# Kernel optimization log

Measured on AMD Instinct MI355X. Metric: run time of the kernel, lower is better.

## Reference

```python
import jax, jax.numpy as jnp
import numpy as np

N_QUBITS = 2
N_LAYERS = 2
EPS = 1e-12  # tf.math.l2_normalize epsilon


def _apply_rx(state, theta, wire):
    """Apply RX(theta) to `wire` of a batched 2-qubit state.
    state: [B,2,2] complex64 (axis1 = qubit0, axis2 = qubit1); theta: [B] float.
    RX(t) = [[cos(t/2), -i sin(t/2)], [-i sin(t/2), cos(t/2)]]
    """
    c = jnp.cos(theta * 0.5)[:, None].astype(state.dtype)
    s = (-1j * jnp.sin(theta * 0.5))[:, None].astype(state.dtype)
    if wire == 0:
        a, b = state[:, 0, :], state[:, 1, :]
        return jnp.stack([c * a + s * b, s * a + c * b], axis=1)
    else:
        a, b = state[:, :, 0], state[:, :, 1]
        return jnp.stack([c * a + s * b, s * a + c * b], axis=2)


def _cnot01(state):
    # CNOT control=0, target=1: flip qubit1 where qubit0 == 1
    return jnp.stack([state[:, 0, :], state[:, 1, ::-1]], axis=1)


def _circuit(angles, weights_q):
    """angles: [B,2] embedding angles; weights_q: [L,2]. Returns [B,2] <Z_i>."""
    B = angles.shape[0]
    state = jnp.zeros((B, 2, 2), dtype=jnp.complex64).at[:, 0, 0].set(1.0)
    # AngleEmbedding (RX rotations, one per wire)
    state = _apply_rx(state, angles[:, 0], 0)
    state = _apply_rx(state, angles[:, 1], 1)
    # BasicEntanglerLayers: RX per wire then single CNOT(0,1) for 2 wires
    for l in range(weights_q.shape[0]):
        state = _apply_rx(state, jnp.broadcast_to(weights_q[l, 0], (B,)), 0)
        state = _apply_rx(state, jnp.broadcast_to(weights_q[l, 1], (B,)), 1)
        state = _cnot01(state)
    probs = (state * jnp.conj(state)).real  # [B,2,2]
    z0 = probs[:, 0, :].sum(-1) - probs[:, 1, :].sum(-1)
    z1 = probs[:, :, 0].sum(-1) - probs[:, :, 1].sum(-1)
    return jnp.stack([z0, z1], axis=-1).astype(jnp.float32)


def setup_inputs() -> dict:
    key = jax.random.key(0)
    k1, k2, k3, k4 = jax.random.split(key, 4)
    B, D = 65536, 1024
    return {
        "x": jax.random.normal(k1, (B, D), dtype=jnp.float32),
        "dense_w": jax.random.normal(k2, (D, N_QUBITS), dtype=jnp.float32) * 0.05,
        "dense_b": jax.random.normal(k3, (N_QUBITS,), dtype=jnp.float32) * 0.05,
        "weights_q": jax.random.normal(k4, (N_LAYERS, N_QUBITS), dtype=jnp.float32) * 0.05,
    }


def reference(x, dense_w, dense_b, weights_q):
    h = x @ dense_w + dense_b  # [B,2]
    # tf.math.l2_normalize(h, axis=-1)
    h = h * jax.lax.rsqrt(jnp.maximum(jnp.sum(h * h, axis=-1, keepdims=True), EPS))
    return _circuit(h, weights_q)  # [B,2]
```

## Files before the change

### kernel.cpp

```cpp
#include <hip/hip_runtime.h>


#define WAVES_PER_BLOCK 4
#define ROWS_PER_WAVE   8
#define ROWS_PER_BLOCK  (WAVES_PER_BLOCK * ROWS_PER_WAVE)

__device__ __forceinline__ float2 run_circuit(float h0, float h1,
                                              const float cw[2][2],
                                              const float sw[2][2]) {
    float inv = rsqrtf(fmaxf(h0 * h0 + h1 * h1, 1e-12f));
    float s0, c0, s1, c1;
    __sincosf(0.5f * h0 * inv, &s0, &c0);
    __sincosf(0.5f * h1 * inv, &s1, &c1);

    float re[2][2], im[2][2];
    re[0][0] = c0 * c1;  im[0][0] = 0.0f;
    re[0][1] = 0.0f;     im[0][1] = -c0 * s1;
    re[1][0] = 0.0f;     im[1][0] = -s0 * c1;
    re[1][1] = -s0 * s1; im[1][1] = 0.0f;

#pragma unroll
    for (int l = 0; l < 2; ++l) {
        {
            float c = cw[l][0], s = sw[l][0];
#pragma unroll
            for (int k = 0; k < 2; ++k) {
                float ar = re[0][k], ai = im[0][k];
                float br = re[1][k], bi = im[1][k];
                re[0][k] = c * ar + s * bi;
                im[0][k] = c * ai - s * br;
                re[1][k] = s * ai + c * br;
                im[1][k] = c * bi - s * ar;
            }
        }
        {
            float c = cw[l][1], s = sw[l][1];
#pragma unroll
            for (int k = 0; k < 2; ++k) {
                float ar = re[k][0], ai = im[k][0];
                float br = re[k][1], bi = im[k][1];
                re[k][0] = c * ar + s * bi;
                im[k][0] = c * ai - s * br;
                re[k][1] = s * ai + c * br;
                im[k][1] = c * bi - s * ar;
            }
        }
        {
            float tr = re[1][0], ti = im[1][0];
            re[1][0] = re[1][1]; im[1][0] = im[1][1];
            re[1][1] = tr;       im[1][1] = ti;
        }
    }

    float p00 = re[0][0] * re[0][0] + im[0][0] * im[0][0];
    float p01 = re[0][1] * re[0][1] + im[0][1] * im[0][1];
    float p10 = re[1][0] * re[1][0] + im[1][0] * im[1][0];
    float p11 = re[1][1] * re[1][1] + im[1][1] * im[1][1];

    float2 z;
    z.x = (p00 + p01) - (p10 + p11);
    z.y = (p00 + p10) - (p01 + p11);
    return z;
}

__global__ __launch_bounds__(256) void qlayer_kernel(
    const float* __restrict__ x,
    const float* __restrict__ w,
    const float* __restrict__ bias,
    const float* __restrict__ wq,
    float* __restrict__ out,
    int B)
{
    const int lane = threadIdx.x & 63;
    const int wave = threadIdx.x >> 6;
    const int rowBase = (blockIdx.x * WAVES_PER_BLOCK + wave) * ROWS_PER_WAVE;
    if (rowBase >= B) return;

    const float4* __restrict__ w4 = (const float4*)w;
    float4 wA[4], wB[4];
#pragma unroll
    for (int j = 0; j < 4; ++j) {
        int f = lane + 64 * j;
        wA[j] = w4[2 * f];
        wB[j] = w4[2 * f + 1];
    }

    const float b0 = bias[0], b1 = bias[1];

    float cw[2][2], sw[2][2];
#pragma unroll
    for (int l = 0; l < 2; ++l) {
#pragma unroll
        for (int q = 0; q < 2; ++q) {
            float t = 0.5f * wq[l * 2 + q];
            __sincosf(t, &sw[l][q], &cw[l][q]);
        }
    }

    float2* __restrict__ out2 = (float2*)out;

#pragma unroll
    for (int r = 0; r < ROWS_PER_WAVE; r += 2) {
        const int rowA = rowBase + r;
        const int rowB = rowA + 1;
        const bool hasB = (rowB < B);
        if (rowA >= B) break;

        const float4* __restrict__ xA = (const float4*)x + (size_t)rowA * 256;
        const float4* __restrict__ xB = (const float4*)x + (size_t)(hasB ? rowB : rowA) * 256;

        float a0 = 0.f, a1 = 0.f, c0s = 0.f, c1s = 0.f;
#pragma unroll
        for (int j = 0; j < 4; ++j) {
            const int f = lane + 64 * j;
            float4 va = xA[f];
            float4 vb = xB[f];
            a0 = fmaf(va.x, wA[j].x, a0); a1 = fmaf(va.x, wA[j].y, a1);
            a0 = fmaf(va.y, wA[j].z, a0); a1 = fmaf(va.y, wA[j].w, a1);
            a0 = fmaf(va.z, wB[j].x, a0); a1 = fmaf(va.z, wB[j].y, a1);
            a0 = fmaf(va.w, wB[j].z, a0); a1 = fmaf(va.w, wB[j].w, a1);
            c0s = fmaf(vb.x, wA[j].x, c0s); c1s = fmaf(vb.x, wA[j].y, c1s);
            c0s = fmaf(vb.y, wA[j].z, c0s); c1s = fmaf(vb.y, wA[j].w, c1s);
            c0s = fmaf(vb.z, wB[j].x, c0s); c1s = fmaf(vb.z, wB[j].y, c1s);
            c0s = fmaf(vb.w, wB[j].z, c0s); c1s = fmaf(vb.w, wB[j].w, c1s);
        }

#pragma unroll
        for (int off = 32; off >= 1; off >>= 1) {
            a0  += __shfl_xor(a0, off, 64);
            a1  += __shfl_xor(a1, off, 64);
            c0s += __shfl_xor(c0s, off, 64);
            c1s += __shfl_xor(c1s, off, 64);
        }

        float2 zA = run_circuit(a0 + b0, a1 + b1, cw, sw);
        float2 zB = run_circuit(c0s + b0, c1s + b1, cw, sw);

        if (lane == 0) {
            out2[rowA] = zA;
            if (hasB) out2[rowB] = zB;
        }
    }
}

extern "C" void kernel_launch(void* const* d_in, const int* in_sizes, int n_in,
                              void* d_out, int out_size, void* d_ws, size_t ws_size,
                              hipStream_t stream) {
    const float* x    = (const float*)d_in[0];
    const float* w    = (const float*)d_in[1];
    const float* bias = (const float*)d_in[2];
    const float* wq   = (const float*)d_in[3];
    float* out = (float*)d_out;

    const int B = in_sizes[0] / 1024;
    const int grid = (B + ROWS_PER_BLOCK - 1) / ROWS_PER_BLOCK;
    qlayer_kernel<<<grid, 256, 0, stream>>>(x, w, bias, wq, out, B);
}
```

Before: 357.3 us.

## Software-pipeline row loads with nontemporal loads and lane-parallel circuit evaluation

For full waves, the row-pair loop is replaced by an explicitly software-pipelined schedule. The next pair of rows is loaded into registers while FMAs run on the current pair, and x loads use nontemporal hints. Four rows are reduced together and each of four lanes evaluates one row's circuit, so the per-lane circuit work is spread instead of repeated. The change raises register pressure and adds code size, but it aims at more memory-level parallelism in this bandwidth-bound streaming kernel.

```diff
diff --git a/kernel.cpp b/kernel.cpp
--- a/kernel.cpp
+++ b/kernel.cpp
@@ -4,6 +4,12 @@
 #define WAVES_PER_BLOCK 4
 #define ROWS_PER_WAVE   8
 #define ROWS_PER_BLOCK  (WAVES_PER_BLOCK * ROWS_PER_WAVE)
+
+typedef float f4 __attribute__((ext_vector_type(4)));
+
+__device__ __forceinline__ f4 ld_nt(const f4* p) {
+    return __builtin_nontemporal_load(p);
+}
 
 __device__ __forceinline__ float2 run_circuit(float h0, float h1,
                                               const float cw[2][2],
@@ -62,6 +68,34 @@
     z.y = (p00 + p10) - (p01 + p11);
     return z;
 }
+
+#define PAIR_FMA(pa, pb, d0, d1, d2, d3)                                   \
+    do {                                                                   \
+        _Pragma("unroll")                                                  \
+        for (int j = 0; j < 4; ++j) {                                      \
+            f4 vA = pa[j];                                                 \
+            f4 vB = pb[j];                                                 \
+            d0 = fmaf(vA.x, wA[j].x, d0); d1 = fmaf(vA.x, wA[j].y, d1);    \
+            d0 = fmaf(vA.y, wA[j].z, d0); d1 = fmaf(vA.y, wA[j].w, d1);    \
+            d0 = fmaf(vA.z, wB[j].x, d0); d1 = fmaf(vA.z, wB[j].y, d1);    \
+            d0 = fmaf(vA.w, wB[j].z, d0); d1 = fmaf(vA.w, wB[j].w, d1);    \
+            d2 = fmaf(vB.x, wA[j].x, d2); d3 = fmaf(vB.x, wA[j].y, d3);    \
+            d2 = fmaf(vB.y, wA[j].z, d2); d3 = fmaf(vB.y, wA[j].w, d3);    \
+            d2 = fmaf(vB.z, wB[j].x, d2); d3 = fmaf(vB.z, wB[j].y, d3);    \
+            d2 = fmaf(vB.w, wB[j].z, d2); d3 = fmaf(vB.w, wB[j].w, d3);    \
+        }                                                                  \
+    } while (0)
+
+#define PAIR_LOAD(pa, pb, row)                                             \
+    do {                                                                   \
+        const f4* __restrict__ xp = x4 + (size_t)(row) * 256;              \
+        _Pragma("unroll")                                                  \
+        for (int j = 0; j < 4; ++j) {                                      \
+            const int f = lane + 64 * j;                                   \
+            pa[j] = ld_nt(xp + f);                                         \
+            pb[j] = ld_nt(xp + 256 + f);                                   \
+        }                                                                  \
+    } while (0)
 
 __global__ __launch_bounds__(256) void qlayer_kernel(
     const float* __restrict__ x,
@@ -76,8 +110,8 @@
     const int rowBase = (blockIdx.x * WAVES_PER_BLOCK + wave) * ROWS_PER_WAVE;
     if (rowBase >= B) return;
 
-    const float4* __restrict__ w4 = (const float4*)w;
-    float4 wA[4], wB[4];
+    const f4* __restrict__ w4 = (const f4*)w;
+    f4 wA[4], wB[4];
 #pragma unroll
     for (int j = 0; j < 4; ++j) {
         int f = lane + 64 * j;
@@ -98,47 +132,119 @@
     }
 
     float2* __restrict__ out2 = (float2*)out;
-
-#pragma unroll
-    for (int r = 0; r < ROWS_PER_WAVE; r += 2) {
-        const int rowA = rowBase + r;
-        const int rowB = rowA + 1;
-        const bool hasB = (rowB < B);
-        if (rowA >= B) break;
-
-        const float4* __restrict__ xA = (const float4*)x + (size_t)rowA * 256;
-        const float4* __restrict__ xB = (const float4*)x + (size_t)(hasB ? rowB : rowA) * 256;
-
-        float a0 = 0.f, a1 = 0.f, c0s = 0.f, c1s = 0.f;
-#pragma unroll
-        for (int j = 0; j < 4; ++j) {
-            const int f = lane + 64 * j;
-            float4 va = xA[f];
-            float4 vb = xB[f];
-            a0 = fmaf(va.x, wA[j].x, a0); a1 = fmaf(va.x, wA[j].y, a1);
-            a0 = fmaf(va.y, wA[j].z, a0); a1 = fmaf(va.y, wA[j].w, a1);
-            a0 = fmaf(va.z, wB[j].x, a0); a1 = fmaf(va.z, wB[j].y, a1);
-            a0 = fmaf(va.w, wB[j].z, a0); a1 = fmaf(va.w, wB[j].w, a1);
-            c0s = fmaf(vb.x, wA[j].x, c0s); c1s = fmaf(vb.x, wA[j].y, c1s);
-            c0s = fmaf(vb.y, wA[j].z, c0s); c1s = fmaf(vb.y, wA[j].w, c1s);
-            c0s = fmaf(vb.z, wB[j].x, c0s); c1s = fmaf(vb.z, wB[j].y, c1s);
-            c0s = fmaf(vb.w, wB[j].z, c0s); c1s = fmaf(vb.w, wB[j].w, c1s);
-        }
-
-#pragma unroll
-        for (int off = 32; off >= 1; off >>= 1) {
-            a0  += __shfl_xor(a0, off, 64);
-            a1  += __shfl_xor(a1, off, 64);
-            c0s += __shfl_xor(c0s, off, 64);
-            c1s += __shfl_xor(c1s, off, 64);
-        }
-
-        float2 zA = run_circuit(a0 + b0, a1 + b1, cw, sw);
-        float2 zB = run_circuit(c0s + b0, c1s + b1, cw, sw);
-
-        if (lane == 0) {
-            out2[rowA] = zA;
-            if (hasB) out2[rowB] = zB;
+    const f4* __restrict__ x4 = (const f4*)x;
+
+    if (rowBase + ROWS_PER_WAVE <= B) {
+        f4 Xa[4], Xb[4], Ya[4], Yb[4];
+
+        PAIR_LOAD(Xa, Xb, rowBase + 0);
+        PAIR_LOAD(Ya, Yb, rowBase + 2);
+
+        {
+            float s0 = 0.f, s1 = 0.f, s2 = 0.f, s3 = 0.f;
+            float s4 = 0.f, s5 = 0.f, s6 = 0.f, s7 = 0.f;
+
+            PAIR_FMA(Xa, Xb, s0, s1, s2, s3);
+            PAIR_LOAD(Xa, Xb, rowBase + 4);
+            PAIR_FMA(Ya, Yb, s4, s5, s6, s7);
+            PAIR_LOAD(Ya, Yb, rowBase + 6);
+
+#pragma unroll
+            for (int off = 32; off >= 1; off >>= 1) {
+                s0 += __shfl_xor(s0, off, 64);
+                s1 += __shfl_xor(s1, off, 64);
+                s2 += __shfl_xor(s2, off, 64);
+                s3 += __shfl_xor(s3, off, 64);
+                s4 += __shfl_xor(s4, off, 64);
+                s5 += __shfl_xor(s5, off, 64);
+                s6 += __shfl_xor(s6, off, 64);
+                s7 += __shfl_xor(s7, off, 64);
+            }
+
+            const int k = lane & 3;
+            float h0 = (k & 1) ? s2 : s0;
+            float h0h = (k & 1) ? s6 : s4;
+            h0 = (k & 2) ? h0h : h0;
+            float h1 = (k & 1) ? s3 : s1;
+            float h1h = (k & 1) ? s7 : s5;
+            h1 = (k & 2) ? h1h : h1;
+
+            float2 z = run_circuit(h0 + b0, h1 + b1, cw, sw);
+            if (lane < 4) out2[rowBase + lane] = z;
+        }
+
+        {
+            float s0 = 0.f, s1 = 0.f, s2 = 0.f, s3 = 0.f;
+            float s4 = 0.f, s5 = 0.f, s6 = 0.f, s7 = 0.f;
+
+            PAIR_FMA(Xa, Xb, s0, s1, s2, s3);
+            PAIR_FMA(Ya, Yb, s4, s5, s6, s7);
+
+#pragma unroll
+            for (int off = 32; off >= 1; off >>= 1) {
+                s0 += __shfl_xor(s0, off, 64);
+                s1 += __shfl_xor(s1, off, 64);
+                s2 += __shfl_xor(s2, off, 64);
+                s3 += __shfl_xor(s3, off, 64);
+                s4 += __shfl_xor(s4, off, 64);
+                s5 += __shfl_xor(s5, off, 64);
+                s6 += __shfl_xor(s6, off, 64);
+                s7 += __shfl_xor(s7, off, 64);
+            }
+
+            const int k = lane & 3;
+            float h0 = (k & 1) ? s2 : s0;
+            float h0h = (k & 1) ? s6 : s4;
+            h0 = (k & 2) ? h0h : h0;
+            float h1 = (k & 1) ? s3 : s1;
+            float h1h = (k & 1) ? s7 : s5;
+            h1 = (k & 2) ? h1h : h1;
+
+            float2 z = run_circuit(h0 + b0, h1 + b1, cw, sw);
+            if (lane < 4) out2[rowBase + 4 + lane] = z;
+        }
+    } else {
+#pragma unroll
+        for (int r = 0; r < ROWS_PER_WAVE; r += 2) {
+            const int rowA = rowBase + r;
+            if (rowA >= B) break;
+            const int rowB = rowA + 1;
+            const bool hasB = (rowB < B);
+
+            const f4* __restrict__ xA = x4 + (size_t)rowA * 256;
+            const f4* __restrict__ xB = x4 + (size_t)(hasB ? rowB : rowA) * 256;
+
+            float a0 = 0.f, a1 = 0.f, c0s = 0.f, c1s = 0.f;
+#pragma unroll
+            for (int j = 0; j < 4; ++j) {
+                const int f = lane + 64 * j;
+                f4 vA = xA[f];
+                f4 vB = xB[f];
+                a0 = fmaf(vA.x, wA[j].x, a0); a1 = fmaf(vA.x, wA[j].y, a1);
+                a0 = fmaf(vA.y, wA[j].z, a0); a1 = fmaf(vA.y, wA[j].w, a1);
+                a0 = fmaf(vA.z, wB[j].x, a0); a1 = fmaf(vA.z, wB[j].y, a1);
+                a0 = fmaf(vA.w, wB[j].z, a0); a1 = fmaf(vA.w, wB[j].w, a1);
+                c0s = fmaf(vB.x, wA[j].x, c0s); c1s = fmaf(vB.x, wA[j].y, c1s);
+                c0s = fmaf(vB.y, wA[j].z, c0s); c1s = fmaf(vB.y, wA[j].w, c1s);
+                c0s = fmaf(vB.z, wB[j].x, c0s); c1s = fmaf(vB.z, wB[j].y, c1s);
+                c0s = fmaf(vB.w, wB[j].z, c0s); c1s = fmaf(vB.w, wB[j].w, c1s);
+            }
+
+#pragma unroll
+            for (int off = 32; off >= 1; off >>= 1) {
+                a0  += __shfl_xor(a0, off, 64);
+                a1  += __shfl_xor(a1, off, 64);
+                c0s += __shfl_xor(c0s, off, 64);
+                c1s += __shfl_xor(c1s, off, 64);
+            }
+
+            float2 zA = run_circuit(a0 + b0, a1 + b1, cw, sw);
+            float2 zB = run_circuit(c0s + b0, c1s + b1, cw, sw);
+
+            if (lane == 0) {
+                out2[rowA] = zA;
+                if (hasB) out2[rowB] = zB;
+            }
         }
     }
 }
```

Measured after the change: 334.0 us (median of 2 runs). 6.5% less time.
